# Kernel tuning notes

Hardware: AMD Instinct MI355X
Metric: run time of the kernel (lower is better)

The kernel has to match this reference:

```python
import jax, jax.numpy as jnp
import numpy as np

K = 7          # kernel_size
PAD = K // 2   # padding


def _unfold(t):
    """im2col for kxk neighborhood: (B,C,H,W) -> (B,C,K*K,H,W), zero-padded."""
    B, C, H, W = t.shape
    p = jnp.pad(t, ((0, 0), (0, 0), (PAD, PAD), (PAD, PAD)))
    # row-major over kernel offsets matches F.unfold ordering
    wins = jnp.stack([p[:, :, i:i + H, j:j + W]
                      for i in range(K) for j in range(K)], axis=2)
    return wins


def setup_inputs() -> dict:
    key = jax.random.key(0)
    ks = jax.random.split(key, 7)
    B, C, H, W = 8, 128, 64, 64
    scale = 1.0 / np.sqrt(C)
    x = jax.random.normal(ks[0], (B, C, H, W), dtype=jnp.float32)
    Wq = jax.random.normal(ks[1], (C, C), dtype=jnp.float32) * scale
    Wk = jax.random.normal(ks[2], (C, C), dtype=jnp.float32) * scale
    Wv = jax.random.normal(ks[3], (C, C), dtype=jnp.float32) * scale
    bq = jax.random.normal(ks[4], (C,), dtype=jnp.float32) * 0.01
    bk = jax.random.normal(ks[5], (C,), dtype=jnp.float32) * 0.01
    bv = jax.random.normal(ks[6], (C,), dtype=jnp.float32) * 0.01
    return {"x": x, "Wq": Wq, "bq": bq, "Wk": Wk, "bk": bk, "Wv": Wv, "bv": bv}


def reference(x, Wq, bq, Wk, bk, Wv, bv):
    # 1x1 convs = channel GEMMs
    q = jnp.einsum('oc,bchw->bohw', Wq, x) + bq[:, None, None]
    k = jnp.einsum('oc,bchw->bohw', Wk, x) + bk[:, None, None]
    v = jnp.einsum('oc,bchw->bohw', Wv, x) + bv[:, None, None]
    k_unf = _unfold(k)   # (B,C,K*K,H,W)
    v_unf = _unfold(v)   # (B,C,K*K,H,W)
    # attention scores over the K*K neighborhood, summed over channels
    attn = jnp.einsum('bchw,bcphw->bphw', q, k_unf)
    attn = jax.nn.softmax(attn, axis=1)
    y = jnp.einsum('bphw,bcphw->bchw', attn, v_unf)
    return y
```

## Files before the change

### kernel.cpp

```cpp
#include <hip/hip_runtime.h>
#include <hip/hip_bf16.h>

#define CC   128
#define HH_  64
#define WW_  64
#define BB   8
#define HWSZ (HH_*WW_)
#define CHW  (CC*HWSZ)
#define BCHW (BB*CHW)
#define PAD  3
#define NP   49

typedef __attribute__((ext_vector_type(8))) short short8;
typedef __attribute__((ext_vector_type(4))) float float4v;

__global__ __launch_bounds__(256) void prep_w(
    const float* __restrict__ Wq, const float* __restrict__ Wk,
    const float* __restrict__ Wv,
    unsigned short* __restrict__ whi, unsigned short* __restrict__ wlo)
{
    int i = blockIdx.x * 256 + threadIdx.x;
    const float* src = (i < 16384) ? Wq : (i < 32768 ? Wk : Wv);
    float f = src[i & 16383];
    __hip_bfloat16 h = __float2bfloat16(f);
    float hf = __bfloat162float(h);
    __hip_bfloat16 l = __float2bfloat16(f - hf);
    unsigned short hu, lu;
    __builtin_memcpy(&hu, &h, 2);
    __builtin_memcpy(&lu, &l, 2);
    whi[i] = hu;
    wlo[i] = lu;
}

__global__ __launch_bounds__(256, 2) void qkv_mfma(
    const float* __restrict__ x,
    const unsigned short* __restrict__ whi, const unsigned short* __restrict__ wlo,
    const float* __restrict__ bq, const float* __restrict__ bk,
    const float* __restrict__ bv, float* __restrict__ qkv)
{
    __shared__ unsigned short xT[2][128][136];
    const int proj = blockIdx.y;
    const int n0g  = blockIdx.x << 7;
    const int b    = n0g >> 12;
    const int npx  = n0g & 4095;
    const int tid  = threadIdx.x;
    const int lane = tid & 63;
    const int wv   = tid >> 6;
    const int wm   = wv & 1, wn = wv >> 1;

    const float* xb = x + (size_t)b*CHW + npx;
    #pragma unroll
    for (int it = 0; it < 16; ++it) {
        int f  = tid + (it << 8);
        int c  = f >> 5;
        int p4 = (f & 31) << 2;
        int csw = (((c >> 3) ^ ((p4 >> 3) & 7)) << 3) | (c & 7);
        float4 v = *(const float4*)&xb[(size_t)c*HWSZ + p4];
        float vv[4] = {v.x, v.y, v.z, v.w};
        #pragma unroll
        for (int u = 0; u < 4; ++u) {
            __hip_bfloat16 h = __float2bfloat16(vv[u]);
            float hf = __bfloat162float(h);
            __hip_bfloat16 l = __float2bfloat16(vv[u] - hf);
            unsigned short hu, lu;
            __builtin_memcpy(&hu, &h, 2);
            __builtin_memcpy(&lu, &l, 2);
            xT[0][p4 + u][csw] = hu;
            xT[1][p4 + u][csw] = lu;
        }
    }

    const float* Bp = (proj == 0) ? bq : (proj == 1 ? bk : bv);
    const int q4 = lane >> 4;
    float4v acc[4][4];
    #pragma unroll
    for (int sm = 0; sm < 4; ++sm) {
        const int mb = wm*64 + sm*16 + q4*4;
        float4v bi;
        bi[0] = Bp[mb+0]; bi[1] = Bp[mb+1]; bi[2] = Bp[mb+2]; bi[3] = Bp[mb+3];
        #pragma unroll
        for (int sn = 0; sn < 4; ++sn) acc[sm][sn] = bi;
    }

    __syncthreads();

    const unsigned short* Wh = whi + (size_t)proj*16384;
    const unsigned short* Wl = wlo + (size_t)proj*16384;
    const int kq8  = q4 << 3;
    const int mrow = lane & 15;

    for (int pass = 0; pass < 3; ++pass) {
        const unsigned short* Wp = (pass == 2) ? Wl : Wh;
        const int xi = (pass == 1) ? 1 : 0;
        #pragma unroll
        for (int kc = 0; kc < 4; ++kc) {
            const int kb = kc << 5;
            short8 a[4], bf[4];
            #pragma unroll
            for (int sm = 0; sm < 4; ++sm) {
                const int m = wm*64 + sm*16 + mrow;
                a[sm] = *(const short8*)&Wp[(size_t)m*CC + kb + kq8];
            }
            #pragma unroll
            for (int sn = 0; sn < 4; ++sn) {
                const int n = wn*64 + sn*16 + mrow;
                const int scol = (kb + kq8) ^ (((n >> 3) & 7) << 3);
                bf[sn] = *(const short8*)&xT[xi][n][scol];
            }
            #pragma unroll
            for (int sm = 0; sm < 4; ++sm)
                #pragma unroll
                for (int sn = 0; sn < 4; ++sn)
                    acc[sm][sn] = __builtin_amdgcn_mfma_f32_16x16x32_bf16(
                        a[sm], bf[sn], acc[sm][sn], 0, 0, 0);
        }
    }

    float* op = qkv + (size_t)proj*BCHW + (size_t)b*CHW + npx;
    #pragma unroll
    for (int sm = 0; sm < 4; ++sm) {
        const int mb = wm*64 + sm*16 + q4*4;
        #pragma unroll
        for (int sn = 0; sn < 4; ++sn) {
            const int n = wn*64 + sn*16 + mrow;
            #pragma unroll
            for (int r = 0; r < 4; ++r)
                op[(size_t)(mb + r)*HWSZ + n] = acc[sm][sn][r];
        }
    }
}

__device__ __forceinline__ void load_chunk8(const float* __restrict__ src,
                                            int h0, int c0, float4* stg) {
    const int tid = threadIdx.x;
    #pragma unroll
    for (int i = 0; i < 4; ++i) {
        int f   = tid + (i << 9);
        int c   = f >> 7;
        int rem = f & 127;
        int r   = rem >> 4;
        int q4  = (rem & 15) << 2;
        int hh  = h0 - PAD + r;
        if ((unsigned)hh < (unsigned)HH_)
            stg[i] = *(const float4*)&src[(size_t)(c0 + c)*HWSZ + hh*WW_ + q4];
        else
            stg[i] = make_float4(0.f, 0.f, 0.f, 0.f);
    }
}

__global__ __launch_bounds__(512) void locatt(
    const float* __restrict__ qkv, float* __restrict__ out)
{
    __shared__ __align__(16) float smem[2*9792];
    __shared__ float lg[2][NP][64];
    __shared__ float dn[2][64];

    const int blk = blockIdx.x;
    const int xs  = blk & 7;
    const int jj  = blk >> 3;
    const int b   = jj >> 2;
    const int h0  = (((xs << 2) | (jj & 3)) << 1);
    const int tid = threadIdx.x;
    const int s   = tid >> 6;
    const int lane = tid & 63;
    const int q16  = lane & 15;
    const int csub = lane >> 4;
    const int w4   = q16 << 2;
    const int w    = lane;

    const float* qp = qkv + (size_t)b*CHW;
    const float* kp = qkv + (size_t)BCHW + (size_t)b*CHW;
    const float* vp = qkv + (size_t)2*BCHW + (size_t)b*CHW;

    {
        int buf = tid >> 8;
        int t2  = tid & 255;
        int idx = t2 & 127;
        int c = idx >> 3, r = idx & 7;
        int col = (t2 < 128) ? 0 : 68;
        *(float4*)&smem[buf*9216 + (c*8 + r)*72 + col] =
            make_float4(0.f, 0.f, 0.f, 0.f);
    }

    const bool do0 = (s < 7);
    const bool do1 = (s >= 1);

    float acc0[7][4], acc1[7][4];
    #pragma unroll
    for (int dx = 0; dx < 7; ++dx)
        #pragma unroll
        for (int j = 0; j < 4; ++j) { acc0[dx][j] = 0.f; acc1[dx][j] = 0.f; }

    float4 stg[4];
    load_chunk8(kp, h0, 0, stg);

    for (int ck = 0; ck < 8; ++ck) {
        float* ksb = smem + (ck & 1)*9216;
        #pragma unroll
        for (int i = 0; i < 4; ++i) {
            int f   = tid + (i << 9);
            int c   = f >> 7;
            int rem = f & 127;
            int r   = rem >> 4;
            int q4  = (rem & 15) << 2;
            *(float4*)&ksb[(c*8 + r)*72 + 4 + q4] = stg[i];
        }
        __syncthreads();
        if (ck < 7) load_chunk8(kp, h0, (ck + 1) * 16, stg);

        const int c0 = ck << 4;
        #pragma unroll
        for (int ci4 = 0; ci4 < 4; ++ci4) {
            const int c = (ci4 << 2) + csub;
            const float* qc = qp + (size_t)(c0 + c)*HWSZ + h0*WW_ + w4;
            float4 q0v = do0 ? *(const float4*)qc
                             : make_float4(0.f, 0.f, 0.f, 0.f);
            float4 q1v = do1 ? *(const float4*)(qc + WW_)
                             : make_float4(0.f, 0.f, 0.f, 0.f);
            const float* krow = &ksb[(c*8 + s)*72];
            float4 ka  = *(const float4*)&krow[w4];
            float4 kb  = *(const float4*)&krow[w4 + 4];
            float4 kc2 = *(const float4*)&krow[w4 + 8];
            float kw[12] = {ka.x,ka.y,ka.z,ka.w, kb.x,kb.y,kb.z,kb.w,
                            kc2.x,kc2.y,kc2.z,kc2.w};
            float q0a[4] = {q0v.x,q0v.y,q0v.z,q0v.w};
            float q1a[4] = {q1v.x,q1v.y,q1v.z,q1v.w};
            #pragma unroll
            for (int dx = 0; dx < 7; ++dx)
                #pragma unroll
                for (int j = 0; j < 4; ++j) {
                    float kv = kw[j + dx + 1];
                    acc0[dx][j] = fmaf(q0a[j], kv, acc0[dx][j]);
                    acc1[dx][j] = fmaf(q1a[j], kv, acc1[dx][j]);
                }
        }
    }

    #pragma unroll
    for (int dx = 0; dx < 7; ++dx)
        #pragma unroll
        for (int j = 0; j < 4; ++j) {
            acc0[dx][j] += __shfl_xor(acc0[dx][j], 16, 64);
            acc0[dx][j] += __shfl_xor(acc0[dx][j], 32, 64);
            acc1[dx][j] += __shfl_xor(acc1[dx][j], 16, 64);
            acc1[dx][j] += __shfl_xor(acc1[dx][j], 32, 64);
        }
    #pragma unroll
    for (int dx = 0; dx < 7; ++dx) {
        if ((dx & 3) == csub) {
            if (do0) *(float4*)&lg[0][s*7 + dx][w4] =
                make_float4(acc0[dx][0], acc0[dx][1], acc0[dx][2], acc0[dx][3]);
            if (do1) *(float4*)&lg[1][(s-1)*7 + dx][w4] =
                make_float4(acc1[dx][0], acc1[dx][1], acc1[dx][2], acc1[dx][3]);
        }
    }

    float vreg[16];
    {
        #pragma unroll
        for (int i = 0; i < 16; ++i) {
            int c  = 2*s + (i >> 3);
            int r  = i & 7;
            int hh = h0 - PAD + r;
            vreg[i] = ((unsigned)hh < (unsigned)HH_)
                      ? vp[(size_t)c*HWSZ + hh*WW_ + w] : 0.f;
        }
    }
    __syncthreads();

    if (tid < 128) {
        const int r = tid >> 6, px = tid & 63;
        float tv[NP];
        float m = -1e30f;
        #pragma unroll
        for (int p = 0; p < NP; ++p) { tv[p] = lg[r][p][px]; m = fmaxf(m, tv[p]); }
        float d = 0.f;
        #pragma unroll
        for (int p = 0; p < NP; ++p) {
            float e = __expf(tv[p] - m);
            d += e;
            lg[r][p][px] = e;
        }
        dn[r][px] = 1.f / d;
    } else {
        int t = tid - 128;
        for (int i = t; i < 2048; i += 384) {
            int buf  = i >> 10;
            int rem1 = i & 1023;
            int r    = rem1 >> 7;
            int rem  = rem1 & 127;
            int colg = rem >> 4;
            int col  = (colg < 4) ? colg : (64 + colg);
            smem[buf*9792 + r*1224 + col*17 + (rem & 15)] = 0.f;
        }
    }
    __syncthreads();

    float a0[NP], a1[NP];
    const float sc0 = dn[0][w], sc1 = dn[1][w];
    #pragma unroll
    for (int p = 0; p < NP; ++p) a0[p] = lg[0][p][w] * sc0;
    #pragma unroll
    for (int p = 0; p < NP; ++p) a1[p] = lg[1][p][w] * sc1;

    for (int ck = 0; ck < 8; ++ck) {
        float* vb = smem + (ck & 1)*9792;
        #pragma unroll
        for (int i = 0; i < 16; ++i) {
            int c = 2*s + (i >> 3);
            int r = i & 7;
            vb[r*1224 + (4 + w)*17 + c] = vreg[i];
        }
        __syncthreads();
        if (ck < 7) {
            int c0v = (ck + 1) << 4;
            #pragma unroll
            for (int i = 0; i < 16; ++i) {
                int c  = 2*s + (i >> 3);
                int r  = i & 7;
                int hh = h0 - PAD + r;
                vreg[i] = ((unsigned)hh < (unsigned)HH_)
                          ? vp[(size_t)(c0v + c)*HWSZ + hh*WW_ + w] : 0.f;
            }
        }
        float y0a = 0.f, y0b = 0.f, y1a = 0.f, y1b = 0.f;
        #pragma unroll
        for (int r = 0; r < 8; ++r) {
            const float* vbase = &vb[r*1224 + (1 + w)*17 + 2*s];
            #pragma unroll
            for (int dx = 0; dx < 7; ++dx) {
                float va = vbase[17*dx];
                float vb2 = vbase[17*dx + 1];
                if (r < 7) {
                    float aw = a0[r*7 + dx];
                    y0a = fmaf(aw, va, y0a); y0b = fmaf(aw, vb2, y0b);
                }
                if (r >= 1) {
                    float aw = a1[(r-1)*7 + dx];
                    y1a = fmaf(aw, va, y1a); y1b = fmaf(aw, vb2, y1b);
                }
            }
        }
        float* op = out + (size_t)b*CHW + (size_t)(ck*16 + 2*s)*HWSZ
                        + (size_t)h0*WW_ + w;
        op[0]          = y0a;
        op[WW_]        = y1a;
        op[HWSZ]       = y0b;
        op[HWSZ + WW_] = y1b;
    }
}

extern "C" void kernel_launch(void* const* d_in, const int* in_sizes, int n_in,
                              void* d_out, int out_size, void* d_ws, size_t ws_size,
                              hipStream_t stream) {
    const float* x  = (const float*)d_in[0];
    const float* Wq = (const float*)d_in[1];
    const float* bq = (const float*)d_in[2];
    const float* Wk = (const float*)d_in[3];
    const float* bk = (const float*)d_in[4];
    const float* Wv = (const float*)d_in[5];
    const float* bv = (const float*)d_in[6];
    float* out = (float*)d_out;
    float* qkv = (float*)d_ws;

    unsigned short* whi = (unsigned short*)d_out;
    unsigned short* wlo = whi + 3*16384;

    prep_w  <<<192, 256, 0, stream>>>(Wq, Wk, Wv, whi, wlo);
    qkv_mfma<<<dim3(256, 3), 256, 0, stream>>>(x, whi, wlo, bq, bk, bv, qkv);
    locatt  <<<256, 512, 0, stream>>>(qkv, out);
}
```

Measured before the change: 136.7 us.

## Drop block barrier in V-accumulate loop and double-buffer staging registers

In the value-aggregation loop, each wave reads only the LDS channel slots it wrote itself, so the per-chunk __syncthreads is replaced with a wave-local s_waitcnt lgkmcnt(0). The K and V global-load staging registers are double-buffered and both chunk loops are fully unrolled, letting next-chunk loads overlap current compute without register reuse stalls. The wave index is also made scalar via readfirstlane so address math can stay in SGPRs. The extra staging registers and unrolling raise VGPR pressure in a 512-thread kernel that already holds 98 attention weights per thread, which risks spills.

```diff
diff --git a/kernel.cpp b/kernel.cpp
--- a/kernel.cpp
+++ b/kernel.cpp
@@ -45,8 +45,8 @@
     const int npx  = n0g & 4095;
     const int tid  = threadIdx.x;
     const int lane = tid & 63;
-    const int wv   = tid >> 6;
-    const int wm   = wv & 1, wn = wv >> 1;
+    const int wvu  = __builtin_amdgcn_readfirstlane(tid >> 6);
+    const int wm   = wvu & 1, wn = wvu >> 1;
 
     const float* xb = x + (size_t)b*CHW + npx;
     #pragma unroll
@@ -161,7 +161,7 @@
     const int b   = jj >> 2;
     const int h0  = (((xs << 2) | (jj & 3)) << 1);
     const int tid = threadIdx.x;
-    const int s   = tid >> 6;
+    const int su  = __builtin_amdgcn_readfirstlane(tid >> 6);
     const int lane = tid & 63;
     const int q16  = lane & 15;
     const int csub = lane >> 4;
@@ -182,8 +182,8 @@
             make_float4(0.f, 0.f, 0.f, 0.f);
     }
 
-    const bool do0 = (s < 7);
-    const bool do1 = (s >= 1);
+    const bool do0 = (su < 7);
+    const bool do1 = (su >= 1);
 
     float acc0[7][4], acc1[7][4];
     #pragma unroll
@@ -191,11 +191,13 @@
         #pragma unroll
         for (int j = 0; j < 4; ++j) { acc0[dx][j] = 0.f; acc1[dx][j] = 0.f; }
 
-    float4 stg[4];
-    load_chunk8(kp, h0, 0, stg);
-
+    float4 stg[2][4];
+    load_chunk8(kp, h0, 0, stg[0]);
+
+    #pragma unroll
     for (int ck = 0; ck < 8; ++ck) {
         float* ksb = smem + (ck & 1)*9216;
+        float4* sc = stg[ck & 1];
         #pragma unroll
         for (int i = 0; i < 4; ++i) {
             int f   = tid + (i << 9);
@@ -203,10 +205,10 @@
             int rem = f & 127;
             int r   = rem >> 4;
             int q4  = (rem & 15) << 2;
-            *(float4*)&ksb[(c*8 + r)*72 + 4 + q4] = stg[i];
+            *(float4*)&ksb[(c*8 + r)*72 + 4 + q4] = sc[i];
         }
         __syncthreads();
-        if (ck < 7) load_chunk8(kp, h0, (ck + 1) * 16, stg);
+        if (ck < 7) load_chunk8(kp, h0, (ck + 1) * 16, stg[(ck + 1) & 1]);
 
         const int c0 = ck << 4;
         #pragma unroll
@@ -217,7 +219,7 @@
                              : make_float4(0.f, 0.f, 0.f, 0.f);
             float4 q1v = do1 ? *(const float4*)(qc + WW_)
                              : make_float4(0.f, 0.f, 0.f, 0.f);
-            const float* krow = &ksb[(c*8 + s)*72];
+            const float* krow = &ksb[(c*8 + su)*72];
             float4 ka  = *(const float4*)&krow[w4];
             float4 kb  = *(const float4*)&krow[w4 + 4];
             float4 kc2 = *(const float4*)&krow[w4 + 8];
@@ -248,22 +250,22 @@
     #pragma unroll
     for (int dx = 0; dx < 7; ++dx) {
         if ((dx & 3) == csub) {
-            if (do0) *(float4*)&lg[0][s*7 + dx][w4] =
+            if (do0) *(float4*)&lg[0][su*7 + dx][w4] =
                 make_float4(acc0[dx][0], acc0[dx][1], acc0[dx][2], acc0[dx][3]);
-            if (do1) *(float4*)&lg[1][(s-1)*7 + dx][w4] =
+            if (do1) *(float4*)&lg[1][(su-1)*7 + dx][w4] =
                 make_float4(acc1[dx][0], acc1[dx][1], acc1[dx][2], acc1[dx][3]);
         }
     }
 
-    float vreg[16];
+    float vreg[2][16];
     {
         #pragma unroll
         for (int i = 0; i < 16; ++i) {
-            int c  = 2*s + (i >> 3);
+            int c  = 2*su + (i >> 3);
             int r  = i & 7;
             int hh = h0 - PAD + r;
-            vreg[i] = ((unsigned)hh < (unsigned)HH_)
-                      ? vp[(size_t)c*HWSZ + hh*WW_ + w] : 0.f;
+            vreg[0][i] = ((unsigned)hh < (unsigned)HH_)
+                         ? vp[(size_t)c*HWSZ + hh*WW_ + w] : 0.f;
         }
     }
     __syncthreads();
@@ -303,33 +305,37 @@
     #pragma unroll
     for (int p = 0; p < NP; ++p) a1[p] = lg[1][p][w] * sc1;
 
+    #pragma unroll
     for (int ck = 0; ck < 8; ++ck) {
         float* vb = smem + (ck & 1)*9792;
+        float* vc = vreg[ck & 1];
         #pragma unroll
         for (int i = 0; i < 16; ++i) {
-            int c = 2*s + (i >> 3);
+            int c = 2*su + (i >> 3);
             int r = i & 7;
-            vb[r*1224 + (4 + w)*17 + c] = vreg[i];
-        }
-        __syncthreads();
+            vb[r*1224 + (4 + w)*17 + c] = vc[i];
+        }
         if (ck < 7) {
             int c0v = (ck + 1) << 4;
+            float* vn = vreg[(ck + 1) & 1];
             #pragma unroll
             for (int i = 0; i < 16; ++i) {
-                int c  = 2*s + (i >> 3);
+                int c  = 2*su + (i >> 3);
                 int r  = i & 7;
                 int hh = h0 - PAD + r;
-                vreg[i] = ((unsigned)hh < (unsigned)HH_)
-                          ? vp[(size_t)(c0v + c)*HWSZ + hh*WW_ + w] : 0.f;
+                vn[i] = ((unsigned)hh < (unsigned)HH_)
+                        ? vp[(size_t)(c0v + c)*HWSZ + hh*WW_ + w] : 0.f;
             }
         }
+        asm volatile("s_waitcnt lgkmcnt(0)" ::: "memory");
+
         float y0a = 0.f, y0b = 0.f, y1a = 0.f, y1b = 0.f;
         #pragma unroll
         for (int r = 0; r < 8; ++r) {
-            const float* vbase = &vb[r*1224 + (1 + w)*17 + 2*s];
+            const float* vbase = &vb[r*1224 + (1 + w)*17 + 2*su];
             #pragma unroll
             for (int dx = 0; dx < 7; ++dx) {
-                float va = vbase[17*dx];
+                float va  = vbase[17*dx];
                 float vb2 = vbase[17*dx + 1];
                 if (r < 7) {
                     float aw = a0[r*7 + dx];
@@ -341,7 +347,7 @@
                 }
             }
         }
-        float* op = out + (size_t)b*CHW + (size_t)(ck*16 + 2*s)*HWSZ
+        float* op = out + (size_t)b*CHW + (size_t)(ck*16 + 2*su)*HWSZ
                         + (size_t)h0*WW_ + w;
         op[0]          = y0a;
         op[WW_]        = y1a;
```

New measurement: 196.5 us. 43.8% more time.
